# Kernel tuning notes

Hardware: AMD Instinct MI355X
Metric: run time of the kernel (lower is better)

The kernel has to match this reference:

```python
import jax, jax.numpy as jnp
import numpy as np

B, T, I, H, L, HPR = 256, 512, 128, 256, 64, 50


def _mlp(x, W1, b1, W2, b2):
    # Linear -> ReLU -> Linear, torch convention y = x @ W.T + b
    return jax.nn.relu(x @ W1.T + b1) @ W2.T + b2


def setup_inputs() -> dict:
    key = jax.random.key(0)
    ks = jax.random.split(key, 16)
    s = 0.05
    return {
        "x": jax.random.uniform(ks[0], (B, T, I), dtype=jnp.float32),
        "hidden": jnp.zeros((B, H), jnp.float32),
        "noise": jax.random.normal(ks[1], (B, T, L), dtype=jnp.float32),
        "Wpm1": s * jax.random.normal(ks[2], (HPR, H)), "bpm1": jnp.zeros((HPR,)),
        "Wpm2": s * jax.random.normal(ks[3], (L, HPR)), "bpm2": jnp.zeros((L,)),
        "Wpl1": s * jax.random.normal(ks[4], (HPR, H)), "bpl1": jnp.zeros((HPR,)),
        "Wpl2": s * jax.random.normal(ks[5], (L, HPR)), "bpl2": jnp.zeros((L,)),
        "Wqm1": s * jax.random.normal(ks[6], (HPR, I + H)), "bqm1": jnp.zeros((HPR,)),
        "Wqm2": s * jax.random.normal(ks[7], (L, HPR)), "bqm2": jnp.zeros((L,)),
        "Wql1": s * jax.random.normal(ks[8], (HPR, I + H)), "bql1": jnp.zeros((HPR,)),
        "Wql2": s * jax.random.normal(ks[9], (L, HPR)), "bql2": jnp.zeros((L,)),
        "Wh1": s * jax.random.normal(ks[10], (HPR, I + H + L)), "bh1": jnp.zeros((HPR,)),
        "Wh2": s * jax.random.normal(ks[11], (H, HPR)), "bh2": jnp.zeros((H,)),
        "Wo": s * jax.random.normal(ks[12], (I, H + L)), "bo": jnp.zeros((I,)),
    }


def reference(x, hidden, noise,
              Wpm1, bpm1, Wpm2, bpm2, Wpl1, bpl1, Wpl2, bpl2,
              Wqm1, bqm1, Wqm2, bqm2, Wql1, bql1, Wql2, bql2,
              Wh1, bh1, Wh2, bh2, Wo, bo):
    def step(h, inp):
        x_t, eps = inp  # [B,I], [B,L]
        xh = jnp.concatenate([x_t, h], axis=1)
        q_mu = _mlp(xh, Wqm1, bqm1, Wqm2, bqm2)
        q_lv = _mlp(xh, Wql1, bql1, Wql2, bql2)
        p_mu = _mlp(h, Wpm1, bpm1, Wpm2, bpm2)
        p_lv = _mlp(h, Wpl1, bpl1, Wpl2, bpl2)
        z = q_mu + jnp.exp(0.5 * q_lv) * eps
        h_next = _mlp(jnp.concatenate([x_t, h, z], axis=1), Wh1, bh1, Wh2, bh2)
        out = jax.nn.sigmoid(jnp.concatenate([h, z], axis=1) @ Wo.T + bo)
        return h_next, (out, p_mu, p_lv, q_mu, q_lv)

    xs = (jnp.swapaxes(x, 0, 1), jnp.swapaxes(noise, 0, 1))  # [T,B,*]
    _, (x_hat, p_mu, p_lv, q_mu, q_lv) = jax.lax.scan(step, hidden, xs)
    tb = lambda a: jnp.swapaxes(a, 0, 1)  # [T,B,*] -> [B,T,*]
    return tb(x_hat), tb(p_mu), tb(p_lv), tb(q_mu), tb(q_lv)
```

## Files before the change

kernel.cpp:

```cpp
#include <hip/hip_runtime.h>
#include <stdint.h>


typedef _Float16 f16x2 __attribute__((ext_vector_type(2)));

__device__ __forceinline__ float bf2f(uint16_t u) {
  union { uint32_t u; float f; } c; c.u = ((uint32_t)u) << 16; return c.f;
}
__device__ __forceinline__ uint16_t f2bf(float f) {
  union { float f; uint32_t u; } c; c.f = f;
  uint32_t u = c.u;
  uint32_t r = (u + 0x7FFFu + ((u >> 16) & 1u)) >> 16;
  return (uint16_t)r;
}
__device__ __forceinline__ uint32_t packh2(float a, float b) {
  union { f16x2 h; uint32_t u; } c;
  c.h.x = (_Float16)a; c.h.y = (_Float16)b; return c.u;
}
__device__ __forceinline__ float fdot2(uint32_t a, uint32_t b, float c) {
  union { uint32_t u; f16x2 h; } ua, ub; ua.u = a; ub.u = b;
#if __has_builtin(__builtin_amdgcn_fdot2)
  return __builtin_amdgcn_fdot2(ua.h, ub.h, c, false);
#else
  return c + (float)ua.h.x * (float)ub.h.x + (float)ua.h.y * (float)ub.h.y;
#endif
}

__device__ __forceinline__ void pin(uint32_t& x) { asm volatile("" : "+v"(x)); }

template <int CTRL>
__device__ __forceinline__ float dpp_mov(float x) {
#if __has_builtin(__builtin_amdgcn_update_dpp)
  union { float f; int i; } a, b;
  a.f = x;
  b.i = __builtin_amdgcn_update_dpp(0, a.i, CTRL, 0xF, 0xF, true);
  return b.f;
#else
  return __shfl_xor(x, (CTRL == 0xB1) ? 1 : (CTRL == 0x4E) ? 2 : 4);
#endif
}
__device__ __forceinline__ float red2(float x) {
  return x + dpp_mov<0xB1>(x);
}
__device__ __forceinline__ float red4(float x) {
  x += dpp_mov<0xB1>(x); x += dpp_mov<0x4E>(x); return x;
}
__device__ __forceinline__ float red8(float x) {
  x += dpp_mov<0xB1>(x); x += dpp_mov<0x4E>(x); x += dpp_mov<0x141>(x); return x;
}

__device__ __forceinline__ void barrier_lds() {
  asm volatile("s_waitcnt lgkmcnt(0)\n\ts_barrier" ::: "memory");
}

__device__ __forceinline__ int sniff_bf16(const uint32_t* xw) {
  int cnt = 0;
#pragma unroll
  for (int i = 0; i < 64; ++i) {
    uint32_t e = (xw[i] >> 7) & 0xFFu;
    cnt += (e >= 0x70u && e <= 0x7Fu) ? 1 : 0;
  }
  return cnt >= 32;
}
__device__ __forceinline__ float loadIn(const void* p, size_t i, int isbf) {
  return isbf ? bf2f(((const uint16_t*)p)[i]) : ((const float*)p)[i];
}
__device__ __forceinline__ void storeOut(void* p, size_t i, float v, int isbf) {
  if (isbf) ((uint16_t*)p)[i] = f2bf(v);
  else      ((float*)p)[i] = v;
}

#define WS_W2   75776
#define WS_BIAS 94208
#define N_JOBS  95168

struct PrepArgs {
  const void* W[11];
  const void* B[11];
  const uint32_t* xw;
};

__global__ void vrnn_prep(PrepArgs a, uint32_t* __restrict__ ws) {
  const int isbf = sniff_bf16(a.xw);
  int j = blockIdx.x * 256 + threadIdx.x;
  if (j < 75776) {
    int p = j >> 9, tid = j & 511;
    int t8 = tid >> 3, c8 = tid & 7;
    const void* W; int row, k, K; bool valid;
    if (p < 24)       { W = a.W[0]; row = t8; k = c8*48 + p*2;        K = 384; valid = row < 50; }
    else if (p < 48)  { W = a.W[1]; row = t8; k = c8*48 + (p-24)*2;   K = 384; valid = row < 50; }
    else if (p < 64)  { W = a.W[2]; row = t8; k = c8*32 + (p-48)*2;   K = 256; valid = row < 50; }
    else if (p < 80)  { W = a.W[3]; row = t8; k = c8*32 + (p-64)*2;   K = 256; valid = row < 50; }
    else if (p < 104) { W = a.W[4]; row = t8; k = c8*48 + (p-80)*2;   K = 448; valid = row < 50; }
    else if (p < 108) { W = a.W[4]; row = t8; k = 384 + c8*8 + (p-104)*2; K = 448; valid = row < 50; }
    else if (p < 124) { W = a.W[5]; row = t8;      k = c8*32 + (p-108)*2;     K = 320; valid = true; }
    else if (p < 128) { W = a.W[5]; row = t8;      k = 256 + c8*8 + (p-124)*2; K = 320; valid = true; }
    else if (p < 144) { W = a.W[5]; row = 64 + t8; k = c8*32 + (p-128)*2;     K = 320; valid = true; }
    else              { W = a.W[5]; row = 64 + t8; k = 256 + c8*8 + (p-144)*2; K = 320; valid = true; }
    float f0 = valid ? loadIn(W, (size_t)row * K + k, isbf)     : 0.f;
    float f1 = valid ? loadIn(W, (size_t)row * K + k + 1, isbf) : 0.f;
    ws[j] = packh2(f0, f1);
  } else if (j < WS_BIAS) {
    int q = j - WS_W2;
    const void* W; int r, kp;
    if (q < 9216) { int m = q / 2304, rem = q % 2304; r = rem / 36; kp = rem % 36; W = a.W[6 + m]; }
    else          { int rem = q - 9216;               r = rem / 36; kp = rem % 36; W = a.W[10]; }
    uint32_t v = 0;
    if (kp < 25) v = packh2(loadIn(W, r * 50 + kp * 2, isbf),
                            loadIn(W, r * 50 + kp * 2 + 1, isbf));
    ws[j] = v;
  } else if (j < N_JOBS) {
    int q = j - WS_BIAS; float v = 0.f;
    if (q < 320)      { int m = q >> 6, i = q & 63; if (i < 50) v = loadIn(a.B[m], i, isbf); }
    else if (q < 576) { int m = (q - 320) >> 6;     v = loadIn(a.B[5 + m], q & 63, isbf); }
    else if (q < 832) { v = loadIn(a.B[9],  q - 576, isbf); }
    else              { v = loadIn(a.B[10], q - 832, isbf); }
    ((float*)ws)[j] = v;
  }
}

__global__ __launch_bounds__(512)
__attribute__((amdgpu_waves_per_eu(2, 2)))
void vrnn_main(
    const void* __restrict__ x, const void* __restrict__ hidden,
    const void* __restrict__ noise, const uint32_t* __restrict__ ws,
    void* __restrict__ out)
{
  __shared__ __align__(16) uint32_t s_w2[18432];
  __shared__ float s_bias[960];
  __shared__ __align__(16) _Float16 s_v[448];
  __shared__ __align__(16) uint32_t s_actu[180];
  _Float16* s_act = (_Float16*)s_actu;

  const int tid = threadIdx.x;
  const int b = blockIdx.x;
  const int isbf = sniff_bf16((const uint32_t*)x);

  uint32_t wqm1[24], wql1[24], wpm1[16], wpl1[16];
  uint32_t wh1a[24], wh1z[4], wo0h[16], wo0z[4], wo1h[16], wo1z[4];
#pragma unroll
  for (int i = 0; i < 24; ++i) { wqm1[i] = ws[(0   + i) * 512 + tid]; pin(wqm1[i]); }
#pragma unroll
  for (int i = 0; i < 24; ++i) { wql1[i] = ws[(24  + i) * 512 + tid]; pin(wql1[i]); }
#pragma unroll
  for (int i = 0; i < 16; ++i) { wpm1[i] = ws[(48  + i) * 512 + tid]; pin(wpm1[i]); }
#pragma unroll
  for (int i = 0; i < 16; ++i) { wpl1[i] = ws[(64  + i) * 512 + tid]; pin(wpl1[i]); }
#pragma unroll
  for (int i = 0; i < 24; ++i) { wh1a[i] = ws[(80  + i) * 512 + tid]; pin(wh1a[i]); }
#pragma unroll
  for (int i = 0; i < 4;  ++i) { wh1z[i] = ws[(104 + i) * 512 + tid]; pin(wh1z[i]); }
#pragma unroll
  for (int i = 0; i < 16; ++i) { wo0h[i] = ws[(108 + i) * 512 + tid]; pin(wo0h[i]); }
#pragma unroll
  for (int i = 0; i < 4;  ++i) { wo0z[i] = ws[(124 + i) * 512 + tid]; pin(wo0z[i]); }
#pragma unroll
  for (int i = 0; i < 16; ++i) { wo1h[i] = ws[(128 + i) * 512 + tid]; pin(wo1h[i]); }
#pragma unroll
  for (int i = 0; i < 4;  ++i) { wo1z[i] = ws[(144 + i) * 512 + tid]; pin(wo1z[i]); }

  for (int i = tid; i < 18432; i += 512) s_w2[i] = ws[WS_W2 + i];
  {
    const float* wsf = (const float*)(ws + WS_BIAS);
    for (int i = tid; i < 960; i += 512) s_bias[i] = wsf[i];
  }

  if (tid < 128)      s_v[tid] = (_Float16)loadIn(x, (size_t)b * 65536 + tid, isbf);
  else if (tid < 384) s_v[tid] = (_Float16)loadIn(hidden, (size_t)b * 256 + (tid - 128), isbf);
  else if (tid < 448) s_v[tid] = (_Float16)0.f;

  const int row8 = tid >> 3, c8 = tid & 7;
  const int i2 = tid >> 2, c4 = tid & 3;
  const int rh = tid >> 1, ch = tid & 1;
  const uint4* v4 = (const uint4*)s_v;

  float eps_r = 0.f;
  if (c4 == 0 && i2 < 64) eps_r = loadIn(noise, (size_t)b * 32768 + i2, isbf);
  float xnext = 0.f;

  __syncthreads();

  const size_t OFF_PMU = 16777216u;
  const size_t OFF_PLV = 25165824u;
  const size_t OFF_QMU = 33554432u;
  const size_t OFF_QLV = 41943040u;

#pragma unroll 1
  for (int t = 0; t < 512; ++t) {
    const size_t bt = (size_t)b * 512 + t;
    if (tid >= 384) {
      int tn = (t < 511) ? t + 1 : 511;
      xnext = loadIn(x, ((size_t)b * 512 + tn) * 128 + (tid - 384), isbf);
    }

    float a_qm = 0.f, a_ql = 0.f, a_hx = 0.f;
    {
      const int g = c8 * 6;
#pragma unroll
      for (int i = 0; i < 6; ++i) {
        uint4 q = v4[g + i];
        a_qm = fdot2(wqm1[4*i+0], q.x, a_qm); a_ql = fdot2(wql1[4*i+0], q.x, a_ql); a_hx = fdot2(wh1a[4*i+0], q.x, a_hx);
        a_qm = fdot2(wqm1[4*i+1], q.y, a_qm); a_ql = fdot2(wql1[4*i+1], q.y, a_ql); a_hx = fdot2(wh1a[4*i+1], q.y, a_hx);
        a_qm = fdot2(wqm1[4*i+2], q.z, a_qm); a_ql = fdot2(wql1[4*i+2], q.z, a_ql); a_hx = fdot2(wh1a[4*i+2], q.z, a_hx);
        a_qm = fdot2(wqm1[4*i+3], q.w, a_qm); a_ql = fdot2(wql1[4*i+3], q.w, a_ql); a_hx = fdot2(wh1a[4*i+3], q.w, a_hx);
      }
    }
    float a_pm = 0.f, a_pl = 0.f, a_o0 = 0.f, a_o1 = 0.f;
    {
      const int g = 16 + c8 * 4;
#pragma unroll
      for (int i = 0; i < 4; ++i) {
        uint4 q = v4[g + i];
        a_pm = fdot2(wpm1[4*i+0], q.x, a_pm); a_pl = fdot2(wpl1[4*i+0], q.x, a_pl);
        a_o0 = fdot2(wo0h[4*i+0], q.x, a_o0); a_o1 = fdot2(wo1h[4*i+0], q.x, a_o1);
        a_pm = fdot2(wpm1[4*i+1], q.y, a_pm); a_pl = fdot2(wpl1[4*i+1], q.y, a_pl);
        a_o0 = fdot2(wo0h[4*i+1], q.y, a_o0); a_o1 = fdot2(wo1h[4*i+1], q.y, a_o1);
        a_pm = fdot2(wpm1[4*i+2], q.z, a_pm); a_pl = fdot2(wpl1[4*i+2], q.z, a_pl);
        a_o0 = fdot2(wo0h[4*i+2], q.z, a_o0); a_o1 = fdot2(wo1h[4*i+2], q.z, a_o1);
        a_pm = fdot2(wpm1[4*i+3], q.w, a_pm); a_pl = fdot2(wpl1[4*i+3], q.w, a_pl);
        a_o0 = fdot2(wo0h[4*i+3], q.w, a_o0); a_o1 = fdot2(wo1h[4*i+3], q.w, a_o1);
      }
    }
    a_qm = red8(a_qm); a_ql = red8(a_ql); a_pm = red8(a_pm); a_pl = red8(a_pl);
    if (c8 == 0) {
      s_act[row8]       = (_Float16)fmaxf(a_qm + s_bias[row8],       0.f);
      s_act[72 + row8]  = (_Float16)fmaxf(a_ql + s_bias[64 + row8],  0.f);
      s_act[144 + row8] = (_Float16)fmaxf(a_pm + s_bias[128 + row8], 0.f);
      s_act[216 + row8] = (_Float16)fmaxf(a_pl + s_bias[192 + row8], 0.f);
    }
    barrier_lds();

    {
      const bool isq = i2 < 64;
      const int r = isq ? i2 : i2 - 64;
      const uint32_t* Wm = s_w2 + (isq ? 0 : 4608) + r * 36 + c4 * 8;
      const uint32_t* Wl = s_w2 + (isq ? 2304 : 6912) + r * 36 + c4 * 8;
      const uint32_t* am = s_actu + (isq ? 0 : 72) + c4 * 8;
      const uint32_t* al = s_actu + (isq ? 36 : 108) + c4 * 8;
      uint4 wm0 = *(const uint4*)Wm, wm1 = *(const uint4*)(Wm + 4);
      uint4 wl0 = *(const uint4*)Wl, wl1 = *(const uint4*)(Wl + 4);
      uint4 am0 = *(const uint4*)am, am1 = *(const uint4*)(am + 4);
      uint4 al0 = *(const uint4*)al, al1 = *(const uint4*)(al + 4);
      float mu0 = 0.f, mu1 = 0.f, lv0 = 0.f, lv1 = 0.f;
      mu0 = fdot2(wm0.x, am0.x, mu0); lv0 = fdot2(wl0.x, al0.x, lv0);
      mu1 = fdot2(wm1.x, am1.x, mu1); lv1 = fdot2(wl1.x, al1.x, lv1);
      mu0 = fdot2(wm0.y, am0.y, mu0); lv0 = fdot2(wl0.y, al0.y, lv0);
      mu1 = fdot2(wm1.y, am1.y, mu1); lv1 = fdot2(wl1.y, al1.y, lv1);
      mu0 = fdot2(wm0.z, am0.z, mu0); lv0 = fdot2(wl0.z, al0.z, lv0);
      mu1 = fdot2(wm1.z, am1.z, mu1); lv1 = fdot2(wl1.z, al1.z, lv1);
      mu0 = fdot2(wm0.w, am0.w, mu0); lv0 = fdot2(wl0.w, al0.w, lv0);
      mu1 = fdot2(wm1.w, am1.w, mu1); lv1 = fdot2(wl1.w, al1.w, lv1);
      float mu = red4(mu0 + mu1);
      float lv = red4(lv0 + lv1);
      if (c4 == 0) {
        mu += s_bias[(isq ? 320 : 448) + r];
        lv += s_bias[(isq ? 384 : 512) + r];
        storeOut(out, (isq ? OFF_QMU : OFF_PMU) + bt * 64 + r, mu, isbf);
        storeOut(out, (isq ? OFF_QLV : OFF_PLV) + bt * 64 + r, lv, isbf);
        if (isq) {
          float z = mu + __expf(0.5f * lv) * eps_r;
          s_v[384 + r] = (_Float16)z;
          int tn = (t < 511) ? t + 1 : 511;
          eps_r = loadIn(noise, ((size_t)b * 512 + tn) * 64 + r, isbf);
        }
      }
    }
    barrier_lds();

    {
      uint4 qz = v4[48 + c8];
      float ah = a_hx, o0 = a_o0, o1 = a_o1;
      ah = fdot2(wh1z[0], qz.x, ah); o0 = fdot2(wo0z[0], qz.x, o0); o1 = fdot2(wo1z[0], qz.x, o1);
      ah = fdot2(wh1z[1], qz.y, ah); o0 = fdot2(wo0z[1], qz.y, o0); o1 = fdot2(wo1z[1], qz.y, o1);
      ah = fdot2(wh1z[2], qz.z, ah); o0 = fdot2(wo0z[2], qz.z, o0); o1 = fdot2(wo1z[2], qz.z, o1);
      ah = fdot2(wh1z[3], qz.w, ah); o0 = fdot2(wo0z[3], qz.w, o0); o1 = fdot2(wo1z[3], qz.w, o1);
      ah = red8(ah); o0 = red8(o0); o1 = red8(o1);
      if (c8 == 0) {
        s_act[288 + row8] = (_Float16)fmaxf(ah + s_bias[256 + row8], 0.f);
        float s0 = 1.f / (1.f + __expf(-(o0 + s_bias[832 + row8])));
        float s1 = 1.f / (1.f + __expf(-(o1 + s_bias[896 + row8])));
        storeOut(out, bt * 128 + row8, s0, isbf);
        storeOut(out, bt * 128 + 64 + row8, s1, isbf);
      }
    }
    barrier_lds();

    {
      const uint32_t* Wr = s_w2 + 9216 + rh * 36 + ch * 16;
      const uint32_t* ap = s_actu + 144 + ch * 16;
      uint4 w0 = *(const uint4*)Wr,        w1 = *(const uint4*)(Wr + 4);
      uint4 w2 = *(const uint4*)(Wr + 8),  w3 = *(const uint4*)(Wr + 12);
      uint4 a0 = *(const uint4*)ap,        a1 = *(const uint4*)(ap + 4);
      uint4 a2 = *(const uint4*)(ap + 8),  a3 = *(const uint4*)(ap + 12);
      float h0 = 0.f, h1 = 0.f;
      h0 = fdot2(w0.x, a0.x, h0); h1 = fdot2(w2.x, a2.x, h1);
      h0 = fdot2(w0.y, a0.y, h0); h1 = fdot2(w2.y, a2.y, h1);
      h0 = fdot2(w0.z, a0.z, h0); h1 = fdot2(w2.z, a2.z, h1);
      h0 = fdot2(w0.w, a0.w, h0); h1 = fdot2(w2.w, a2.w, h1);
      h0 = fdot2(w1.x, a1.x, h0); h1 = fdot2(w3.x, a3.x, h1);
      h0 = fdot2(w1.y, a1.y, h0); h1 = fdot2(w3.y, a3.y, h1);
      h0 = fdot2(w1.z, a1.z, h0); h1 = fdot2(w3.z, a3.z, h1);
      h0 = fdot2(w1.w, a1.w, h0); h1 = fdot2(w3.w, a3.w, h1);
      float hh = red2(h0 + h1);
      if (ch == 0) s_v[128 + rh] = (_Float16)(hh + s_bias[576 + rh]);
    }
    if (tid >= 384) s_v[tid - 384] = (_Float16)xnext;
    barrier_lds();
  }
}

extern "C" void kernel_launch(void* const* d_in, const int* in_sizes, int n_in,
                              void* d_out, int out_size, void* d_ws, size_t ws_size,
                              hipStream_t stream) {
  (void)in_sizes; (void)n_in; (void)out_size; (void)ws_size;
  PrepArgs a;
  a.W[0]  = d_in[11];
  a.W[1]  = d_in[15];
  a.W[2]  = d_in[3];
  a.W[3]  = d_in[7];
  a.W[4]  = d_in[19];
  a.W[5]  = d_in[23];
  a.W[6]  = d_in[13];
  a.W[7]  = d_in[17];
  a.W[8]  = d_in[5];
  a.W[9]  = d_in[9];
  a.W[10] = d_in[21];
  a.B[0]  = d_in[12];
  a.B[1]  = d_in[16];
  a.B[2]  = d_in[4];
  a.B[3]  = d_in[8];
  a.B[4]  = d_in[20];
  a.B[5]  = d_in[14];
  a.B[6]  = d_in[18];
  a.B[7]  = d_in[6];
  a.B[8]  = d_in[10];
  a.B[9]  = d_in[22];
  a.B[10] = d_in[24];
  a.xw    = (const uint32_t*)d_in[0];

  uint32_t* ws = (uint32_t*)d_ws;
  vrnn_prep<<<dim3((N_JOBS + 255) / 256), dim3(256), 0, stream>>>(a, ws);
  vrnn_main<<<dim3(256), dim3(512), 0, stream>>>(d_in[0], d_in[1], d_in[2], ws, d_out);
}
```

Before: 1.258 ms.

## Move prior and output heads off the recurrent critical path into a post kernel

```diff
diff --git a/kernel.cpp b/kernel.cpp
--- a/kernel.cpp
+++ b/kernel.cpp
@@ -69,10 +69,28 @@
   if (isbf) ((uint16_t*)p)[i] = f2bf(v);
   else      ((float*)p)[i] = v;
 }
+__device__ __forceinline__ void parkStore(void* p, size_t i, float v, int isbf) {
+  if (isbf) {
+    union { _Float16 h; uint16_t u; } c; c.h = (_Float16)v;
+    ((uint16_t*)p)[i] = c.u;
+  } else ((float*)p)[i] = v;
+}
+__device__ __forceinline__ _Float16 parkLoadH(const void* p, size_t i, int isbf) {
+  if (isbf) {
+    union { uint16_t u; _Float16 h; } c; c.u = ((const uint16_t*)p)[i];
+    return c.h;
+  }
+  return (_Float16)((const float*)p)[i];
+}
 
 #define WS_W2   75776
 #define WS_BIAS 94208
 #define N_JOBS  95168
+
+#define OFF_PMU 16777216u
+#define OFF_PLV 25165824u
+#define OFF_QMU 33554432u
+#define OFF_QLV 41943040u
 
 struct PrepArgs {
   const void* W[11];
@@ -126,7 +144,6 @@
     const void* __restrict__ noise, const uint32_t* __restrict__ ws,
     void* __restrict__ out)
 {
-  __shared__ __align__(16) uint32_t s_w2[18432];
   __shared__ float s_bias[960];
   __shared__ __align__(16) _Float16 s_v[448];
   __shared__ __align__(16) uint32_t s_actu[180];
@@ -136,30 +153,30 @@
   const int b = blockIdx.x;
   const int isbf = sniff_bf16((const uint32_t*)x);
 
-  uint32_t wqm1[24], wql1[24], wpm1[16], wpl1[16];
-  uint32_t wh1a[24], wh1z[4], wo0h[16], wo0z[4], wo1h[16], wo1z[4];
+  const int row8 = tid >> 3, c8 = tid & 7;
+  const int i2 = tid >> 2, c4 = tid & 3;
+  const int rh = tid >> 1, ch = tid & 1;
+
+  uint32_t wqm1[24], wql1[24], wh1a[24], wh1z[4];
 #pragma unroll
   for (int i = 0; i < 24; ++i) { wqm1[i] = ws[(0   + i) * 512 + tid]; pin(wqm1[i]); }
 #pragma unroll
   for (int i = 0; i < 24; ++i) { wql1[i] = ws[(24  + i) * 512 + tid]; pin(wql1[i]); }
 #pragma unroll
-  for (int i = 0; i < 16; ++i) { wpm1[i] = ws[(48  + i) * 512 + tid]; pin(wpm1[i]); }
-#pragma unroll
-  for (int i = 0; i < 16; ++i) { wpl1[i] = ws[(64  + i) * 512 + tid]; pin(wpl1[i]); }
-#pragma unroll
   for (int i = 0; i < 24; ++i) { wh1a[i] = ws[(80  + i) * 512 + tid]; pin(wh1a[i]); }
 #pragma unroll
   for (int i = 0; i < 4;  ++i) { wh1z[i] = ws[(104 + i) * 512 + tid]; pin(wh1z[i]); }
-#pragma unroll
-  for (int i = 0; i < 16; ++i) { wo0h[i] = ws[(108 + i) * 512 + tid]; pin(wo0h[i]); }
-#pragma unroll
-  for (int i = 0; i < 4;  ++i) { wo0z[i] = ws[(124 + i) * 512 + tid]; pin(wo0z[i]); }
-#pragma unroll
-  for (int i = 0; i < 16; ++i) { wo1h[i] = ws[(128 + i) * 512 + tid]; pin(wo1h[i]); }
-#pragma unroll
-  for (int i = 0; i < 4;  ++i) { wo1z[i] = ws[(144 + i) * 512 + tid]; pin(wo1z[i]); }
-
-  for (int i = tid; i < 18432; i += 512) s_w2[i] = ws[WS_W2 + i];
+
+  const int r2 = i2 & 63;
+  uint32_t q2wm[8], q2wl[8];
+#pragma unroll
+  for (int j = 0; j < 8; ++j) { q2wm[j] = ws[WS_W2 + r2*36 + c4*8 + j];        pin(q2wm[j]); }
+#pragma unroll
+  for (int j = 0; j < 8; ++j) { q2wl[j] = ws[WS_W2 + 2304 + r2*36 + c4*8 + j]; pin(q2wl[j]); }
+  uint32_t p4w[16];
+#pragma unroll
+  for (int j = 0; j < 16; ++j) { p4w[j] = ws[WS_W2 + 9216 + rh*36 + ch*16 + j]; pin(p4w[j]); }
+
   {
     const float* wsf = (const float*)(ws + WS_BIAS);
     for (int i = tid; i < 960; i += 512) s_bias[i] = wsf[i];
@@ -169,21 +186,15 @@
   else if (tid < 384) s_v[tid] = (_Float16)loadIn(hidden, (size_t)b * 256 + (tid - 128), isbf);
   else if (tid < 448) s_v[tid] = (_Float16)0.f;
 
-  const int row8 = tid >> 3, c8 = tid & 7;
-  const int i2 = tid >> 2, c4 = tid & 3;
-  const int rh = tid >> 1, ch = tid & 1;
   const uint4* v4 = (const uint4*)s_v;
 
   float eps_r = 0.f;
   if (c4 == 0 && i2 < 64) eps_r = loadIn(noise, (size_t)b * 32768 + i2, isbf);
   float xnext = 0.f;
+  float hprev = 0.f;
+  if (ch == 0) hprev = loadIn(hidden, (size_t)b * 256 + rh, isbf);
 
   __syncthreads();
-
-  const size_t OFF_PMU = 16777216u;
-  const size_t OFF_PLV = 25165824u;
-  const size_t OFF_QMU = 33554432u;
-  const size_t OFF_QLV = 41943040u;
 
 #pragma unroll 1
   for (int t = 0; t < 512; ++t) {
@@ -191,6 +202,12 @@
     if (tid >= 384) {
       int tn = (t < 511) ? t + 1 : 511;
       xnext = loadIn(x, ((size_t)b * 512 + tn) * 128 + (tid - 384), isbf);
+    }
+    if (ch == 0) {
+      size_t pidx = (rh < 64)  ? OFF_PMU + bt * 64 + rh
+                  : (rh < 128) ? OFF_PLV + bt * 64 + (rh - 64)
+                               : bt * 128 + (rh - 128);
+      parkStore(out, pidx, hprev, isbf);
     }
 
     float a_qm = 0.f, a_ql = 0.f, a_hx = 0.f;
@@ -205,12 +222,147 @@
         a_qm = fdot2(wqm1[4*i+3], q.w, a_qm); a_ql = fdot2(wql1[4*i+3], q.w, a_ql); a_hx = fdot2(wh1a[4*i+3], q.w, a_hx);
       }
     }
+    a_qm = red8(a_qm); a_ql = red8(a_ql);
+    if (c8 == 0) {
+      s_act[row8]      = (_Float16)fmaxf(a_qm + s_bias[row8],      0.f);
+      s_act[72 + row8] = (_Float16)fmaxf(a_ql + s_bias[64 + row8], 0.f);
+    }
+    barrier_lds();
+
+    if (tid < 256) {
+      uint4 am0 = *(const uint4*)(s_actu + c4*8),      am1 = *(const uint4*)(s_actu + c4*8 + 4);
+      uint4 al0 = *(const uint4*)(s_actu + 36 + c4*8), al1 = *(const uint4*)(s_actu + 36 + c4*8 + 4);
+      float mu0 = 0.f, mu1 = 0.f, lv0 = 0.f, lv1 = 0.f;
+      mu0 = fdot2(q2wm[0], am0.x, mu0); lv0 = fdot2(q2wl[0], al0.x, lv0);
+      mu1 = fdot2(q2wm[4], am1.x, mu1); lv1 = fdot2(q2wl[4], al1.x, lv1);
+      mu0 = fdot2(q2wm[1], am0.y, mu0); lv0 = fdot2(q2wl[1], al0.y, lv0);
+      mu1 = fdot2(q2wm[5], am1.y, mu1); lv1 = fdot2(q2wl[5], al1.y, lv1);
+      mu0 = fdot2(q2wm[2], am0.z, mu0); lv0 = fdot2(q2wl[2], al0.z, lv0);
+      mu1 = fdot2(q2wm[6], am1.z, mu1); lv1 = fdot2(q2wl[6], al1.z, lv1);
+      mu0 = fdot2(q2wm[3], am0.w, mu0); lv0 = fdot2(q2wl[3], al0.w, lv0);
+      mu1 = fdot2(q2wm[7], am1.w, mu1); lv1 = fdot2(q2wl[7], al1.w, lv1);
+      float mu = red4(mu0 + mu1);
+      float lv = red4(lv0 + lv1);
+      if (c4 == 0) {
+        mu += s_bias[320 + r2];
+        lv += s_bias[384 + r2];
+        storeOut(out, OFF_QMU + bt * 64 + r2, mu, isbf);
+        storeOut(out, OFF_QLV + bt * 64 + r2, lv, isbf);
+        float z = mu + __expf(0.5f * lv) * eps_r;
+        s_v[384 + r2] = (_Float16)z;
+        int tn = (t < 511) ? t + 1 : 511;
+        eps_r = loadIn(noise, ((size_t)b * 512 + tn) * 64 + r2, isbf);
+      }
+    }
+    barrier_lds();
+
+    {
+      uint4 qz = v4[48 + c8];
+      float ah = a_hx;
+      ah = fdot2(wh1z[0], qz.x, ah);
+      ah = fdot2(wh1z[1], qz.y, ah);
+      ah = fdot2(wh1z[2], qz.z, ah);
+      ah = fdot2(wh1z[3], qz.w, ah);
+      ah = red8(ah);
+      if (c8 == 0)
+        s_act[288 + row8] = (_Float16)fmaxf(ah + s_bias[256 + row8], 0.f);
+    }
+    barrier_lds();
+
+    {
+      const uint32_t* ap = s_actu + 144 + ch * 16;
+      uint4 a0 = *(const uint4*)ap,        a1 = *(const uint4*)(ap + 4);
+      uint4 a2 = *(const uint4*)(ap + 8),  a3 = *(const uint4*)(ap + 12);
+      float h0 = 0.f, h1 = 0.f;
+      h0 = fdot2(p4w[0],  a0.x, h0); h1 = fdot2(p4w[8],  a2.x, h1);
+      h0 = fdot2(p4w[1],  a0.y, h0); h1 = fdot2(p4w[9],  a2.y, h1);
+      h0 = fdot2(p4w[2],  a0.z, h0); h1 = fdot2(p4w[10], a2.z, h1);
+      h0 = fdot2(p4w[3],  a0.w, h0); h1 = fdot2(p4w[11], a2.w, h1);
+      h0 = fdot2(p4w[4],  a1.x, h0); h1 = fdot2(p4w[12], a3.x, h1);
+      h0 = fdot2(p4w[5],  a1.y, h0); h1 = fdot2(p4w[13], a3.y, h1);
+      h0 = fdot2(p4w[6],  a1.z, h0); h1 = fdot2(p4w[14], a3.z, h1);
+      h0 = fdot2(p4w[7],  a1.w, h0); h1 = fdot2(p4w[15], a3.w, h1);
+      float hh = red2(h0 + h1);
+      if (ch == 0) {
+        float hv = hh + s_bias[576 + rh];
+        s_v[128 + rh] = (_Float16)hv;
+        hprev = hv;
+      }
+    }
+    if (tid >= 384) s_v[tid - 384] = (_Float16)xnext;
+    barrier_lds();
+  }
+}
+
+__global__ __launch_bounds__(512)
+__attribute__((amdgpu_waves_per_eu(2, 2)))
+void vrnn_post(
+    const void* __restrict__ x, const void* __restrict__ noise,
+    const uint32_t* __restrict__ ws, void* __restrict__ out)
+{
+  __shared__ float s_bias[960];
+  __shared__ __align__(16) _Float16 s_v[448];
+  __shared__ __align__(16) uint32_t s_actu[180];
+  _Float16* s_act = (_Float16*)s_actu;
+
+  const int tid = threadIdx.x;
+  const int isbf = sniff_bf16((const uint32_t*)x);
+
+  const int row8 = tid >> 3, c8 = tid & 7;
+  const int c4 = tid & 3;
+  const int gid = tid >> 2;
+  const int mp = gid >> 6, rr = gid & 63;
+
+  uint32_t wpm1[16], wpl1[16], wo0h[16], wo0z[4], wo1h[16], wo1z[4];
+#pragma unroll
+  for (int i = 0; i < 16; ++i) { wpm1[i] = ws[(48  + i) * 512 + tid]; pin(wpm1[i]); }
+#pragma unroll
+  for (int i = 0; i < 16; ++i) { wpl1[i] = ws[(64  + i) * 512 + tid]; pin(wpl1[i]); }
+#pragma unroll
+  for (int i = 0; i < 16; ++i) { wo0h[i] = ws[(108 + i) * 512 + tid]; pin(wo0h[i]); }
+#pragma unroll
+  for (int i = 0; i < 4;  ++i) { wo0z[i] = ws[(124 + i) * 512 + tid]; pin(wo0z[i]); }
+#pragma unroll
+  for (int i = 0; i < 16; ++i) { wo1h[i] = ws[(128 + i) * 512 + tid]; pin(wo1h[i]); }
+#pragma unroll
+  for (int i = 0; i < 4;  ++i) { wo1z[i] = ws[(144 + i) * 512 + tid]; pin(wo1z[i]); }
+  uint32_t pw[8];
+#pragma unroll
+  for (int j = 0; j < 8; ++j) { pw[j] = ws[WS_W2 + (mp ? 6912 : 4608) + rr*36 + c4*8 + j]; pin(pw[j]); }
+
+  {
+    const float* wsf = (const float*)(ws + WS_BIAS);
+    for (int i = tid; i < 960; i += 512) s_bias[i] = wsf[i];
+  }
+  __syncthreads();
+
+  const uint4* v4 = (const uint4*)s_v;
+
+#pragma unroll 1
+  for (int it = 0; it < 64; ++it) {
+    const size_t g = (size_t)blockIdx.x * 64 + it;
+
+    if (tid < 256) {
+      int r = tid;
+      size_t pidx = (r < 64)  ? OFF_PMU + g * 64 + r
+                  : (r < 128) ? OFF_PLV + g * 64 + (r - 64)
+                              : g * 128 + (r - 128);
+      s_v[128 + r] = parkLoadH(out, pidx, isbf);
+    } else if (tid < 320) {
+      int r = tid - 256;
+      float mu  = loadIn(out, OFF_QMU + g * 64 + r, isbf);
+      float lv  = loadIn(out, OFF_QLV + g * 64 + r, isbf);
+      float eps = loadIn(noise, g * 64 + r, isbf);
+      s_v[384 + r] = (_Float16)(mu + __expf(0.5f * lv) * eps);
+    }
+    barrier_lds();
+
     float a_pm = 0.f, a_pl = 0.f, a_o0 = 0.f, a_o1 = 0.f;
     {
-      const int g = 16 + c8 * 4;
+      const int gg = 16 + c8 * 4;
 #pragma unroll
       for (int i = 0; i < 4; ++i) {
-        uint4 q = v4[g + i];
+        uint4 q = v4[gg + i];
         a_pm = fdot2(wpm1[4*i+0], q.x, a_pm); a_pl = fdot2(wpl1[4*i+0], q.x, a_pl);
         a_o0 = fdot2(wo0h[4*i+0], q.x, a_o0); a_o1 = fdot2(wo1h[4*i+0], q.x, a_o1);
         a_pm = fdot2(wpm1[4*i+1], q.y, a_pm); a_pl = fdot2(wpl1[4*i+1], q.y, a_pl);
@@ -220,91 +372,37 @@
         a_pm = fdot2(wpm1[4*i+3], q.w, a_pm); a_pl = fdot2(wpl1[4*i+3], q.w, a_pl);
         a_o0 = fdot2(wo0h[4*i+3], q.w, a_o0); a_o1 = fdot2(wo1h[4*i+3], q.w, a_o1);
       }
-    }
-    a_qm = red8(a_qm); a_ql = red8(a_ql); a_pm = red8(a_pm); a_pl = red8(a_pl);
+      uint4 qz = v4[48 + c8];
+      a_o0 = fdot2(wo0z[0], qz.x, a_o0); a_o1 = fdot2(wo1z[0], qz.x, a_o1);
+      a_o0 = fdot2(wo0z[1], qz.y, a_o0); a_o1 = fdot2(wo1z[1], qz.y, a_o1);
+      a_o0 = fdot2(wo0z[2], qz.z, a_o0); a_o1 = fdot2(wo1z[2], qz.z, a_o1);
+      a_o0 = fdot2(wo0z[3], qz.w, a_o0); a_o1 = fdot2(wo1z[3], qz.w, a_o1);
+    }
+    a_pm = red8(a_pm); a_pl = red8(a_pl); a_o0 = red8(a_o0); a_o1 = red8(a_o1);
     if (c8 == 0) {
-      s_act[row8]       = (_Float16)fmaxf(a_qm + s_bias[row8],       0.f);
-      s_act[72 + row8]  = (_Float16)fmaxf(a_ql + s_bias[64 + row8],  0.f);
       s_act[144 + row8] = (_Float16)fmaxf(a_pm + s_bias[128 + row8], 0.f);
       s_act[216 + row8] = (_Float16)fmaxf(a_pl + s_bias[192 + row8], 0.f);
+      float s0 = 1.f / (1.f + __expf(-(a_o0 + s_bias[832 + row8])));
+      float s1 = 1.f / (1.f + __expf(-(a_o1 + s_bias[896 + row8])));
+      storeOut(out, g * 128 + row8, s0, isbf);
+      storeOut(out, g * 128 + 64 + row8, s1, isbf);
     }
     barrier_lds();
 
     {
-      const bool isq = i2 < 64;
-      const int r = isq ? i2 : i2 - 64;
-      const uint32_t* Wm = s_w2 + (isq ? 0 : 4608) + r * 36 + c4 * 8;
-      const uint32_t* Wl = s_w2 + (isq ? 2304 : 6912) + r * 36 + c4 * 8;
-      const uint32_t* am = s_actu + (isq ? 0 : 72) + c4 * 8;
-      const uint32_t* al = s_actu + (isq ? 36 : 108) + c4 * 8;
-      uint4 wm0 = *(const uint4*)Wm, wm1 = *(const uint4*)(Wm + 4);
-      uint4 wl0 = *(const uint4*)Wl, wl1 = *(const uint4*)(Wl + 4);
-      uint4 am0 = *(const uint4*)am, am1 = *(const uint4*)(am + 4);
-      uint4 al0 = *(const uint4*)al, al1 = *(const uint4*)(al + 4);
-      float mu0 = 0.f, mu1 = 0.f, lv0 = 0.f, lv1 = 0.f;
-      mu0 = fdot2(wm0.x, am0.x, mu0); lv0 = fdot2(wl0.x, al0.x, lv0);
-      mu1 = fdot2(wm1.x, am1.x, mu1); lv1 = fdot2(wl1.x, al1.x, lv1);
-      mu0 = fdot2(wm0.y, am0.y, mu0); lv0 = fdot2(wl0.y, al0.y, lv0);
-      mu1 = fdot2(wm1.y, am1.y, mu1); lv1 = fdot2(wl1.y, al1.y, lv1);
-      mu0 = fdot2(wm0.z, am0.z, mu0); lv0 = fdot2(wl0.z, al0.z, lv0);
-      mu1 = fdot2(wm1.z, am1.z, mu1); lv1 = fdot2(wl1.z, al1.z, lv1);
-      mu0 = fdot2(wm0.w, am0.w, mu0); lv0 = fdot2(wl0.w, al0.w, lv0);
-      mu1 = fdot2(wm1.w, am1.w, mu1); lv1 = fdot2(wl1.w, al1.w, lv1);
-      float mu = red4(mu0 + mu1);
-      float lv = red4(lv0 + lv1);
+      const uint32_t* ab = s_actu + (mp ? 108 : 72) + c4 * 8;
+      uint4 a0 = *(const uint4*)ab, a1 = *(const uint4*)(ab + 4);
+      float v0 = 0.f, v1 = 0.f;
+      v0 = fdot2(pw[0], a0.x, v0); v1 = fdot2(pw[4], a1.x, v1);
+      v0 = fdot2(pw[1], a0.y, v0); v1 = fdot2(pw[5], a1.y, v1);
+      v0 = fdot2(pw[2], a0.z, v0); v1 = fdot2(pw[6], a1.z, v1);
+      v0 = fdot2(pw[3], a0.w, v0); v1 = fdot2(pw[7], a1.w, v1);
+      float v = red4(v0 + v1);
       if (c4 == 0) {
-        mu += s_bias[(isq ? 320 : 448) + r];
-        lv += s_bias[(isq ? 384 : 512) + r];
-        storeOut(out, (isq ? OFF_QMU : OFF_PMU) + bt * 64 + r, mu, isbf);
-        storeOut(out, (isq ? OFF_QLV : OFF_PLV) + bt * 64 + r, lv, isbf);
-        if (isq) {
-          float z = mu + __expf(0.5f * lv) * eps_r;
-          s_v[384 + r] = (_Float16)z;
-          int tn = (t < 511) ? t + 1 : 511;
-          eps_r = loadIn(noise, ((size_t)b * 512 + tn) * 64 + r, isbf);
-        }
+        v += s_bias[(mp ? 512 : 448) + rr];
+        storeOut(out, (mp ? OFF_PLV : OFF_PMU) + g * 64 + rr, v, isbf);
       }
     }
-    barrier_lds();
-
-    {
-      uint4 qz = v4[48 + c8];
-      float ah = a_hx, o0 = a_o0, o1 = a_o1;
-      ah = fdot2(wh1z[0], qz.x, ah); o0 = fdot2(wo0z[0], qz.x, o0); o1 = fdot2(wo1z[0], qz.x, o1);
-      ah = fdot2(wh1z[1], qz.y, ah); o0 = fdot2(wo0z[1], qz.y, o0); o1 = fdot2(wo1z[1], qz.y, o1);
-      ah = fdot2(wh1z[2], qz.z, ah); o0 = fdot2(wo0z[2], qz.z, o0); o1 = fdot2(wo1z[2], qz.z, o1);
-      ah = fdot2(wh1z[3], qz.w, ah); o0 = fdot2(wo0z[3], qz.w, o0); o1 = fdot2(wo1z[3], qz.w, o1);
-      ah = red8(ah); o0 = red8(o0); o1 = red8(o1);
-      if (c8 == 0) {
-        s_act[288 + row8] = (_Float16)fmaxf(ah + s_bias[256 + row8], 0.f);
-        float s0 = 1.f / (1.f + __expf(-(o0 + s_bias[832 + row8])));
-        float s1 = 1.f / (1.f + __expf(-(o1 + s_bias[896 + row8])));
-        storeOut(out, bt * 128 + row8, s0, isbf);
-        storeOut(out, bt * 128 + 64 + row8, s1, isbf);
-      }
-    }
-    barrier_lds();
-
-    {
-      const uint32_t* Wr = s_w2 + 9216 + rh * 36 + ch * 16;
-      const uint32_t* ap = s_actu + 144 + ch * 16;
-      uint4 w0 = *(const uint4*)Wr,        w1 = *(const uint4*)(Wr + 4);
-      uint4 w2 = *(const uint4*)(Wr + 8),  w3 = *(const uint4*)(Wr + 12);
-      uint4 a0 = *(const uint4*)ap,        a1 = *(const uint4*)(ap + 4);
-      uint4 a2 = *(const uint4*)(ap + 8),  a3 = *(const uint4*)(ap + 12);
-      float h0 = 0.f, h1 = 0.f;
-      h0 = fdot2(w0.x, a0.x, h0); h1 = fdot2(w2.x, a2.x, h1);
-      h0 = fdot2(w0.y, a0.y, h0); h1 = fdot2(w2.y, a2.y, h1);
-      h0 = fdot2(w0.z, a0.z, h0); h1 = fdot2(w2.z, a2.z, h1);
-      h0 = fdot2(w0.w, a0.w, h0); h1 = fdot2(w2.w, a2.w, h1);
-      h0 = fdot2(w1.x, a1.x, h0); h1 = fdot2(w3.x, a3.x, h1);
-      h0 = fdot2(w1.y, a1.y, h0); h1 = fdot2(w3.y, a3.y, h1);
-      h0 = fdot2(w1.z, a1.z, h0); h1 = fdot2(w3.z, a3.z, h1);
-      h0 = fdot2(w1.w, a1.w, h0); h1 = fdot2(w3.w, a3.w, h1);
-      float hh = red2(h0 + h1);
-      if (ch == 0) s_v[128 + rh] = (_Float16)(hh + s_bias[576 + rh]);
-    }
-    if (tid >= 384) s_v[tid - 384] = (_Float16)xnext;
     barrier_lds();
   }
 }
@@ -341,4 +439,5 @@
   uint32_t* ws = (uint32_t*)d_ws;
   vrnn_prep<<<dim3((N_JOBS + 255) / 256), dim3(256), 0, stream>>>(a, ws);
   vrnn_main<<<dim3(256), dim3(512), 0, stream>>>(d_in[0], d_in[1], d_in[2], ws, d_out);
-}
+  vrnn_post<<<dim3(2048), dim3(512), 0, stream>>>(d_in[0], d_in[2], ws, d_out);
+}
```

Result: slower. 1.920 ms (+52.6%).
